# Kernel tuning notes

Hardware: AMD Instinct MI355X
Metric: run time of the kernel (lower is better)

The kernel has to match this reference:

```python
import jax, jax.numpy as jnp
import numpy as np

SHORT = 2000
CUTVALS = [0, 2000, 12000, 40000, 100000]  # [0] + cutoffs + [n_classes]
OSZ = [10000, 28000, 60000]
HSZ = [384, 192, 96]
IN_F = 768
LN_EPS = 1e-5


def setup_inputs() -> dict:
    key = jax.random.key(0)
    ks = jax.random.split(key, 16)
    B, L = 256, 20
    inp = {
        "x": jax.random.normal(ks[0], (B, IN_F), jnp.float32),
        "head_W": jax.random.normal(ks[1], (SHORT + 3, IN_F), jnp.float32) / np.sqrt(IN_F),
        "target": jax.random.randint(ks[2], (B, L), 0, CUTVALS[-1], jnp.int64)
        if jax.config.jax_enable_x64 else jax.random.randint(ks[2], (B, L), 0, CUTVALS[-1], jnp.int32),
    }
    for i in range(3):
        inp[f"w1_{i}"] = jax.random.normal(ks[3 + 4 * i], (HSZ[i], IN_F), jnp.float32) / np.sqrt(IN_F)
        inp[f"g{i}"] = jnp.ones((HSZ[i],), jnp.float32)
        inp[f"b{i}"] = jnp.zeros((HSZ[i],), jnp.float32)
        inp[f"w2_{i}"] = jax.random.normal(ks[4 + 4 * i], (OSZ[i], HSZ[i]), jnp.float32) / np.sqrt(HSZ[i])
    return inp


def _bce_with_logits(logits, y):
    # matches torch BCEWithLogitsLoss(reduction='none')
    return jnp.maximum(logits, 0.0) - logits * y + jnp.log1p(jnp.exp(-jnp.abs(logits)))


def reference(x, head_W, w1_0, g0, b0, w2_0, w1_1, g1, b1, w2_1, w1_2, g2, b2, w2_2, target):
    W1, G, Bp, W2 = [w1_0, w1_1, w1_2], [g0, g1, g2], [b0, b1, b2], [w2_0, w2_1, w2_2]
    B = x.shape[0]
    rows = jnp.arange(B)[:, None]
    dt = x.dtype

    head_logits = x @ head_W.T  # [B, SHORT + n_clusters]

    # shortlist multi-hot (rows with no shortlist label stay all-zero, as in torch)
    m0 = target < SHORT
    onehot_short = jnp.zeros((B, SHORT), dt).at[rows, jnp.clip(target, 0, SHORT - 1)].max(m0.astype(dt))

    total_cluster = jnp.zeros((B,), dt)
    actives = []
    for i in range(3):
        low, high = CUTVALS[i + 1], CUTVALS[i + 2]
        osz = high - low
        m = (target >= low) & (target < high)  # [B, L]
        active = m.any(axis=1).astype(dt)      # [B]
        actives.append(active)
        # multi-hot targets for this cluster
        y = jnp.zeros((B, osz), dt).at[rows, jnp.clip(target - low, 0, osz - 1)].max(m.astype(dt))
        # tail projection: Linear -> LayerNorm -> ReLU -> Linear
        h = x @ W1[i].T
        mu = h.mean(-1, keepdims=True)
        var = ((h - mu) ** 2).mean(-1, keepdims=True)
        h = jax.nn.relu((h - mu) * jax.lax.rsqrt(var + LN_EPS) * G[i] + Bp[i])
        # p = sigmoid(cluster-root logit) * sigmoid(tail logits)
        root = jax.nn.sigmoid(head_logits[:, SHORT + i])[:, None]  # [B,1]
        p = root * jax.nn.sigmoid(h @ W2[i].T)                     # [B, osz]
        # torch BCELoss clamps log at -100
        bce = -(y * jnp.maximum(jnp.log(p), -100.0) + (1.0 - y) * jnp.maximum(jnp.log1p(-p), -100.0))
        total_cluster = total_cluster + active * bce.sum(axis=1)

    cluster_onehot = jnp.stack(actives, axis=1)  # [B, 3]
    head_y = jnp.concatenate([onehot_short, cluster_onehot], axis=1)
    head_loss = _bce_with_logits(head_logits, head_y)  # [B, SHORT+3]
    mult = (cluster_onehot == 0).astype(dt)
    head_loss = jnp.concatenate([head_loss[:, :SHORT], head_loss[:, SHORT:] * mult], axis=1)
    head_loss = head_loss.sum(axis=1)

    csz = jnp.asarray(OSZ, dt)
    num_loss = (mult + cluster_onehot * csz).sum(axis=1) + SHORT
    return ((head_loss + total_cluster) / num_loss).mean()
```

## Files before the change

### kernel.cpp

```cpp
#include <hip/hip_runtime.h>
#include <hip/hip_bf16.h>

#define INF 768
#define NSHORT 2000
#define NHEAD 2003

typedef __attribute__((ext_vector_type(8))) short  s16x8;
typedef __attribute__((ext_vector_type(4))) float  f32x4;
typedef __attribute__((ext_vector_type(8))) float  f32x8;

__device__ __forceinline__ float sigf(float z) { return 1.f / (1.f + __expf(-z)); }
__device__ __forceinline__ float softplusf(float z) {
    return fmaxf(z, 0.f) + __logf(1.f + __expf(-fabsf(z)));
}
__device__ __forceinline__ float qreduce16(float v) {
    v += __shfl_xor(v, 1); v += __shfl_xor(v, 2);
    v += __shfl_xor(v, 4); v += __shfl_xor(v, 8);
    return v;
}
__device__ __forceinline__ float wreduce64(float v) {
    v += __shfl_xor(v, 1);  v += __shfl_xor(v, 2);  v += __shfl_xor(v, 4);
    v += __shfl_xor(v, 8);  v += __shfl_xor(v, 16); v += __shfl_xor(v, 32);
    return v;
}
__device__ __forceinline__ short bfc(float x) {
    union { __hip_bfloat16 h; short s; } u; u.h = __float2bfloat16(x); return u.s;
}

template <int K32, int KC, int MODE, int AF32>
__device__ __forceinline__ void core_c(
    const void* __restrict__ Av, int kbase32,
    const float* __restrict__ W, int Kfull, int N, int stripe,
    short* __restrict__ lds,
    float* __restrict__ outH, int ldH,
    float* __restrict__ part, int pslot,
    const float* __restrict__ rootlogit, int ci)
{
    constexpr int NCH = K32 / KC;
    const int t = threadIdx.x;
    const int wave = t >> 6, lane = t & 63;
    const int quad = lane >> 4, l16 = lane & 15;
    const int rtb = wave * 4;

    const int sct = t >> 6, sl = t & 63;
    int scol = stripe * 64 + sct * 16 + (sl & 15);
    if (scol >= N) scol = N - 1;
    const float* wsrc = W + (size_t)scol * Kfull + kbase32 * 32 + (sl >> 4) * 8;

    size_t aoff[4];
#pragma unroll
    for (int rt = 0; rt < 4; rt++) {
        if (AF32)
            aoff[rt] = (size_t)((rtb + rt) * 16 + l16) * Kfull + kbase32 * 32 + quad * 8;
        else
            aoff[rt] = (size_t)(rtb + rt) * K32 * 512 + (size_t)lane * 8;
    }

#pragma unroll
    for (int s = 0; s < KC; s++) {
        const f32x8 v = *(const f32x8*)(wsrc + (size_t)s * 32);
        s16x8 o;
#pragma unroll
        for (int i = 0; i < 8; i++) o[i] = bfc(v[i]);
        *(s16x8*)(lds + (((size_t)s * 4 + sct) * 64 + sl) * 8) = o;
    }
    __syncthreads();

    f32x4 acc[4][4];
#pragma unroll
    for (int rt = 0; rt < 4; rt++)
#pragma unroll
        for (int ct = 0; ct < 4; ct++) acc[rt][ct] = (f32x4){0.f, 0.f, 0.f, 0.f};

#pragma unroll
    for (int c = 0; c < NCH; c++) {
        short* lbuf = lds + (size_t)(c & 1) * (KC * 2048);
        f32x8 nv[KC];
        if (c + 1 < NCH) {
#pragma unroll
            for (int s = 0; s < KC; s++)
                nv[s] = *(const f32x8*)(wsrc + ((size_t)((c + 1) * KC + s)) * 32);
        }
#pragma unroll
        for (int jj = 0; jj < KC; jj++) {
            const int jg = c * KC + jj;
            s16x8 af[4];
            if (AF32) {
#pragma unroll
                for (int rt = 0; rt < 4; rt++) {
                    const f32x8 v = *(const f32x8*)((const float*)Av + aoff[rt] + (size_t)jg * 32);
#pragma unroll
                    for (int i = 0; i < 8; i++) af[rt][i] = bfc(v[i]);
                }
            } else {
#pragma unroll
                for (int rt = 0; rt < 4; rt++)
                    af[rt] = *(const s16x8*)((const short*)Av + aoff[rt] + (size_t)jg * 512);
            }
#pragma unroll
            for (int ct = 0; ct < 4; ct++) {
                const s16x8 wf = *(const s16x8*)(lbuf + (((size_t)jj * 4 + ct) * 64 + lane) * 8);
#pragma unroll
                for (int rt = 0; rt < 4; rt++)
                    acc[rt][ct] = __builtin_amdgcn_mfma_f32_16x16x32_bf16(
                        af[rt], wf, acc[rt][ct], 0, 0, 0);
            }
        }
        if (c + 1 < NCH) {
            short* nbuf = lds + (size_t)((c + 1) & 1) * (KC * 2048);
            __syncthreads();
#pragma unroll
            for (int s = 0; s < KC; s++) {
                s16x8 o;
#pragma unroll
                for (int i = 0; i < 8; i++) o[i] = bfc(nv[s][i]);
                *(s16x8*)(nbuf + (((size_t)s * 4 + sct) * 64 + sl) * 8) = o;
            }
            __syncthreads();
        }
    }

    const int col0 = stripe * 64;
    if (MODE == 0) {
#pragma unroll
        for (int rt = 0; rt < 4; rt++)
#pragma unroll
            for (int ct = 0; ct < 4; ct++) {
                const int col = col0 + ct * 16 + l16;
                if (col < N) {
#pragma unroll
                    for (int r = 0; r < 4; r++)
                        outH[(size_t)((rtb + rt) * 16 + quad * 4 + r) * ldH + col] =
                            acc[rt][ct][r];
                }
            }
    } else if (MODE == 1) {
#pragma unroll
        for (int rt = 0; rt < 4; rt++) {
#pragma unroll
            for (int r = 0; r < 4; r++) {
                const int row = (rtb + rt) * 16 + quad * 4 + r;
                float m = 0.f, Pp = 1.f;
#pragma unroll
                for (int ct = 0; ct < 4; ct++) {
                    const int col = col0 + ct * 16 + l16;
                    if (col < NSHORT) {
                        const float z = acc[rt][ct][r];
                        m += fmaxf(z, 0.f);
                        Pp *= 1.f + __expf(-fabsf(z));
                    }
                }
                float s = m + __logf(Pp);
                s = qreduce16(s);
                if (l16 == 0) part[(size_t)pslot * 256 + row] = s;
            }
        }
    } else {
#pragma unroll
        for (int rt = 0; rt < 4; rt++) {
#pragma unroll
            for (int r = 0; r < 4; r++) {
                const int row = (rtb + rt) * 16 + quad * 4 + r;
                const float rv = sigf(rootlogit[row * 3 + ci]);
                float pd = 1.f, pn = 1.f;
#pragma unroll
                for (int ct = 0; ct < 4; ct++) {
                    const int col = col0 + ct * 16 + l16;
                    const float tv = fminf(__expf(-acc[rt][ct][r]), 1e6f);
                    const float d = (col < N) ? (1.f + tv) : 1.f;
                    const float n = (col < N) ? (1.f + tv - rv) : 1.f;
                    pd *= d; pn *= n;
                }
                float s = __logf(pd) - __logf(pn);
                s = qreduce16(s);
                if (l16 == 0) part[(size_t)pslot * 256 + row] = s;
            }
        }
    }
}

template <int K32>
__device__ __forceinline__ void core_b(
    const __hip_bfloat16* __restrict__ Ap,
    const float* __restrict__ W, int N, int stripe,
    short* __restrict__ lds,
    float* __restrict__ part, int pslot,
    const float* __restrict__ rootlogit, int ci)
{
    const int t = threadIdx.x;
    const int wave = t >> 6, lane = t & 63;
    const int quad = lane >> 4, l16 = lane & 15;
    const int rtb = wave * 4;
    const int Kfull = K32 * 32;

    const int sct = t >> 6, sl = t & 63;
    int scol = stripe * 64 + sct * 16 + (sl & 15);
    if (scol >= N) scol = N - 1;
    const float* wsrc = W + (size_t)scol * Kfull + (sl >> 4) * 8;
    short* wdst = lds + ((size_t)sct * 64 + sl) * 8;

    constexpr int G = (K32 <= 6) ? K32 : 6;
    constexpr int NG = K32 / G;
    f32x8 buf[G];
#pragma unroll
    for (int s = 0; s < G; s++) buf[s] = *(const f32x8*)(wsrc + (size_t)s * 32);
#pragma unroll
    for (int gg = 0; gg < NG; gg++) {
        f32x8 nbuf[G];
        if (gg + 1 < NG) {
#pragma unroll
            for (int s = 0; s < G; s++)
                nbuf[s] = *(const f32x8*)(wsrc + (size_t)((gg + 1) * G + s) * 32);
        }
#pragma unroll
        for (int s = 0; s < G; s++) {
            s16x8 o;
#pragma unroll
            for (int i = 0; i < 8; i++) o[i] = bfc(buf[s][i]);
            *(s16x8*)(wdst + (size_t)(gg * G + s) * 2048) = o;
        }
        if (gg + 1 < NG) {
#pragma unroll
            for (int s = 0; s < G; s++) buf[s] = nbuf[s];
        }
    }
    __syncthreads();

    const short* abase = (const short*)Ap + (size_t)lane * 8;
    f32x4 acc[4][4];
#pragma unroll
    for (int rt = 0; rt < 4; rt++)
#pragma unroll
        for (int ct = 0; ct < 4; ct++) acc[rt][ct] = (f32x4){0.f, 0.f, 0.f, 0.f};

#pragma unroll
    for (int j = 0; j < K32; j++) {
        s16x8 af[4];
#pragma unroll
        for (int rt = 0; rt < 4; rt++)
            af[rt] = *(const s16x8*)(abase + (size_t)((rtb + rt) * K32 + j) * 512);
#pragma unroll
        for (int ct = 0; ct < 4; ct++) {
            const s16x8 wf = *(const s16x8*)(lds + (((size_t)j * 4 + ct) * 64 + lane) * 8);
#pragma unroll
            for (int rt = 0; rt < 4; rt++)
                acc[rt][ct] = __builtin_amdgcn_mfma_f32_16x16x32_bf16(
                    af[rt], wf, acc[rt][ct], 0, 0, 0);
        }
    }

    const int col0 = stripe * 64;
#pragma unroll
    for (int rt = 0; rt < 4; rt++) {
#pragma unroll
        for (int r = 0; r < 4; r++) {
            const int row = (rtb + rt) * 16 + quad * 4 + r;
            const float rv = sigf(rootlogit[row * 3 + ci]);
            float pd = 1.f, pn = 1.f;
#pragma unroll
            for (int ct = 0; ct < 4; ct++) {
                const int col = col0 + ct * 16 + l16;
                const float tv = fminf(__expf(-acc[rt][ct][r]), 1e6f);
                const float d = (col < N) ? (1.f + tv) : 1.f;
                const float n = (col < N) ? (1.f + tv - rv) : 1.f;
                pd *= d; pn *= n;
            }
            float s = __logf(pd) - __logf(pn);
            s = qreduce16(s);
            if (l16 == 0) part[(size_t)pslot * 256 + row] = s;
        }
    }
}

__global__ __launch_bounds__(256) void k_mm1(
    const float* __restrict__ x, const float* __restrict__ headW,
    const float* __restrict__ w10, const float* __restrict__ w11,
    const float* __restrict__ w12,
    float* __restrict__ phead,
    float* h0, float* h1, float* h2,
    float* __restrict__ rootlogit)
{
    __shared__ __align__(16) short smem[16384];
    const int bx = blockIdx.x;
    if (bx < 32) {
        core_c<24, 4, 1, 1>(x, 0, headW, INF, NHEAD, bx, smem,
                            nullptr, 0, phead, bx, nullptr, 0);
    } else if (bx < 38) {
        core_c<24, 4, 0, 1>(x, 0, w10, INF, 384, bx - 32, smem,
                            h0, 384, nullptr, 0, nullptr, 0);
    } else if (bx < 41) {
        core_c<24, 4, 0, 1>(x, 0, w11, INF, 192, bx - 38, smem,
                            h1, 192, nullptr, 0, nullptr, 0);
    } else if (bx < 43) {
        core_c<24, 4, 0, 1>(x, 0, w12, INF, 96, bx - 41, smem,
                            h2, 96, nullptr, 0, nullptr, 0);
    } else {
        const int row = bx - 43, wave = threadIdx.x >> 6, lane = threadIdx.x & 63;
        if (wave < 3) {
            const float* xr = x + row * INF;
            const float* wr = headW + (size_t)(NSHORT + wave) * INF;
            float s = 0.f;
            for (int k = lane; k < INF; k += 64) s += xr[k] * wr[k];
            s = wreduce64(s);
            if (lane == 0) rootlogit[row * 3 + wave] = s;
        }
    }
}

__global__ __launch_bounds__(256) void k_ln(const float* h0, const float* h1, const float* h2,
                                            const float* g0, const float* g1, const float* g2,
                                            const float* b0, const float* b1, const float* b2,
                                            __hip_bfloat16* f0, __hip_bfloat16* f1,
                                            __hip_bfloat16* f2,
                                            __hip_bfloat16* p0, __hip_bfloat16* p1,
                                            __hip_bfloat16* p2,
                                            float* __restrict__ out) {
    if (blockIdx.x == 0 && threadIdx.x == 0) out[0] = 0.f;
    const int task = blockIdx.x * 4 + (threadIdx.x >> 6);
    const int ci = task >> 8, row = task & 255, lane = threadIdx.x & 63;
    const float *h, *g, *bb; __hip_bfloat16 *fo, *po; int hsz, K32;
    if (ci == 0)      { h = h0; g = g0; bb = b0; fo = f0; po = p0; hsz = 384; K32 = 12; }
    else if (ci == 1) { h = h1; g = g1; bb = b1; fo = f1; po = p1; hsz = 192; K32 = 6; }
    else              { h = h2; g = g2; bb = b2; fo = f2; po = p2; hsz = 96;  K32 = 3; }
    const float* hr = h + (size_t)row * hsz;
    float s = 0.f, s2 = 0.f;
    for (int k = lane; k < hsz; k += 64) { const float v = hr[k]; s += v; s2 += v * v; }
    s = wreduce64(s); s2 = wreduce64(s2);
    const float mu = s / hsz;
    const float var = s2 / hsz - mu * mu;
    const float rsn = rsqrtf(var + 1e-5f);
    const int nch = hsz >> 3;
    if (lane < nch) {
        const f32x8 v = *(const f32x8*)(hr + lane * 8);
        const f32x8 gg = *(const f32x8*)(g + lane * 8);
        const f32x8 bv = *(const f32x8*)(bb + lane * 8);
        s16x8 o;
#pragma unroll
        for (int i = 0; i < 8; i++)
            o[i] = bfc(fmaxf((v[i] - mu) * rsn * gg[i] + bv[i], 0.f));
        *(s16x8*)((short*)fo + (size_t)row * hsz + lane * 8) = o;
        const size_t chunk = ((size_t)(row >> 4) * K32 + (lane >> 2)) * 64
                           + (lane & 3) * 16 + (row & 15);
        *(s16x8*)((short*)po + chunk * 8) = o;
    }
}

__global__ __launch_bounds__(256) void k_bce(const __hip_bfloat16* p0,
                                             const __hip_bfloat16* p1,
                                             const __hip_bfloat16* p2,
                                             const float* __restrict__ w20,
                                             const float* __restrict__ w21,
                                             const float* __restrict__ w22,
                                             float* __restrict__ part,
                                             const float* __restrict__ rootlogit) {
    __shared__ __align__(16) short smem[24576];
    const int s = blockIdx.x;
    if (s < 157)
        core_b<12>(p0, w20, 10000, s, smem, part, s, rootlogit, 0);
    else if (s < 595)
        core_b<6>(p1, w21, 28000, s - 157, smem, part, s, rootlogit, 1);
    else
        core_b<3>(p2, w22, 60000, s - 595, smem, part, s, rootlogit, 2);
}

__global__ __launch_bounds__(256) void k_red(const float* __restrict__ part,
                                             const float* __restrict__ phead,
                                             const float* __restrict__ rootlogit,
                                             const int* __restrict__ target,
                                             const float* __restrict__ x,
                                             const float* __restrict__ headW,
                                             const __hip_bfloat16* f0,
                                             const __hip_bfloat16* f1,
                                             const __hip_bfloat16* f2,
                                             const float* w20, const float* w21, const float* w22,
                                             float* __restrict__ out) {
    const int row = blockIdx.x;
    const int t = threadIdx.x, wave = t >> 6, lane = t & 63;
    __shared__ float sx[INF];
    __shared__ __hip_bfloat16 shb[384 + 192 + 96];
    __shared__ int st[20];
    __shared__ float scorr[4];
    __shared__ float red[4][4];
    for (int i = t; i < INF; i += 256) sx[i] = x[row * INF + i];
    for (int i = t; i < 384; i += 256) shb[i] = f0[row * 384 + i];
    for (int i = t; i < 192; i += 256) shb[384 + i] = f1[row * 192 + i];
    for (int i = t; i < 96; i += 256)  shb[576 + i] = f2[row * 96 + i];
    if (t < 20) st[t] = target[row * 20 + t];
    if (t < 4) scorr[t] = 0.f;
    __syncthreads();
    for (int l = wave; l < 20; l += 4) {
        const int tg = st[l];
        bool dup = false;
        for (int m = 0; m < l; m++) dup |= (st[m] == tg);
        if (dup) continue;
        if (tg < NSHORT) {
            const float* wr = headW + (size_t)tg * INF;
            float z = 0.f;
            for (int k = lane; k < INF; k += 64) z += sx[k] * wr[k];
            z = wreduce64(z);
            if (lane == 0) atomicAdd(&scorr[3], -z);
        } else {
            int ci, low, hsz, hoff; const float* w2;
            if (tg < 12000)      { ci = 0; low = 2000;  hsz = 384; hoff = 0;   w2 = w20; }
            else if (tg < 40000) { ci = 1; low = 12000; hsz = 192; hoff = 384; w2 = w21; }
            else                 { ci = 2; low = 40000; hsz = 96;  hoff = 576; w2 = w22; }
            const float* wr = w2 + (size_t)(tg - low) * hsz;
            float z = 0.f;
            for (int k = lane; k < hsz; k += 64)
                z += __bfloat162float(shb[hoff + k]) * wr[k];
            z = wreduce64(z);
            if (lane == 0) {
                const float rvv = sigf(rootlogit[row * 3 + ci]);
                const float p = rvv * sigf(z);
                atomicAdd(&scorr[ci],
                          -fmaxf(__logf(p), -100.f) + fmaxf(__logf(1.f - p), -100.f));
            }
        }
    }
    float c0 = 0.f, c1 = 0.f, c2 = 0.f, hs = 0.f;
    for (int i = t; i < 1533; i += 256) {
        const float v = part[(size_t)i * 256 + row];
        if (i < 157) c0 += v; else if (i < 595) c1 += v; else c2 += v;
    }
    if (t < 32) hs = phead[(size_t)t * 256 + row];
    c0 = wreduce64(c0); c1 = wreduce64(c1); c2 = wreduce64(c2); hs = wreduce64(hs);
    if (lane == 0) { red[0][wave] = c0; red[1][wave] = c1; red[2][wave] = c2; red[3][wave] = hs; }
    __syncthreads();
    if (t == 0) {
        float cc[3];
        for (int i = 0; i < 3; i++) cc[i] = red[i][0] + red[i][1] + red[i][2] + red[i][3];
        float hsum = red[3][0] + red[3][1] + red[3][2] + red[3][3] + scorr[3];
        bool act[3] = {false, false, false};
        for (int l = 0; l < 20; l++) {
            const int tg = target[row * 20 + l];
            if (tg >= 2000) {
                if (tg < 12000) act[0] = true;
                else if (tg < 40000) act[1] = true;
                else act[2] = true;
            }
        }
        float total = 0.f, num = 2000.f;
        const float csz[3] = {10000.f, 28000.f, 60000.f};
        for (int i = 0; i < 3; i++) {
            if (act[i]) { total += cc[i] + scorr[i]; num += csz[i]; }
            else        { hsum += softplusf(rootlogit[row * 3 + i]); num += 1.f; }
        }
        atomicAdd(out, (hsum + total) / num * (1.f / 256.f));
    }
}

extern "C" void kernel_launch(void* const* d_in, const int* in_sizes, int n_in,
                              void* d_out, int out_size, void* d_ws, size_t ws_size,
                              hipStream_t stream) {
    const float* x      = (const float*)d_in[0];
    const float* headW  = (const float*)d_in[1];
    const int*   target = (const int*)d_in[2];
    const float* w10 = (const float*)d_in[3];
    const float* g0  = (const float*)d_in[4];
    const float* b0  = (const float*)d_in[5];
    const float* w20 = (const float*)d_in[6];
    const float* w11 = (const float*)d_in[7];
    const float* g1  = (const float*)d_in[8];
    const float* b1  = (const float*)d_in[9];
    const float* w21 = (const float*)d_in[10];
    const float* w12 = (const float*)d_in[11];
    const float* g2  = (const float*)d_in[12];
    const float* b2  = (const float*)d_in[13];
    const float* w22 = (const float*)d_in[14];
    float* out = (float*)d_out;

    char* ws = (char*)d_ws;
    size_t off = 0;
    auto carve = [&](size_t bytes) -> void* {
        void* p = ws + off;
        off += (bytes + 255) & ~(size_t)255;
        return p;
    };
    float* h0            = (float*)carve((size_t)256 * 384 * 4);
    float* h1            = (float*)carve((size_t)256 * 192 * 4);
    float* h2            = (float*)carve((size_t)256 * 96 * 4);
    __hip_bfloat16* f0   = (__hip_bfloat16*)carve((size_t)256 * 384 * 2);
    __hip_bfloat16* f1   = (__hip_bfloat16*)carve((size_t)256 * 192 * 2);
    __hip_bfloat16* f2   = (__hip_bfloat16*)carve((size_t)256 * 96 * 2);
    __hip_bfloat16* p0   = (__hip_bfloat16*)carve((size_t)256 * 384 * 2);
    __hip_bfloat16* p1   = (__hip_bfloat16*)carve((size_t)256 * 192 * 2);
    __hip_bfloat16* p2   = (__hip_bfloat16*)carve((size_t)256 * 96 * 2);
    float* rootlogit     = (float*)carve((size_t)256 * 3 * 4);
    float* phead         = (float*)carve((size_t)32 * 256 * 4);
    float* part          = (float*)carve((size_t)1536 * 256 * 4);

    k_mm1<<<299, 256, 0, stream>>>(x, headW, w10, w11, w12,
                                   phead, h0, h1, h2, rootlogit);
    k_ln<<<192, 256, 0, stream>>>(h0, h1, h2, g0, g1, g2, b0, b1, b2,
                                  f0, f1, f2, p0, p1, p2, out);
    k_bce<<<1533, 256, 0, stream>>>(p0, p1, p2, w20, w21, w22, part, rootlogit);
    k_red<<<256, 256, 0, stream>>>(part, phead, rootlogit, target, x, headW,
                                   f0, f1, f2, w20, w21, w22, out);

    (void)in_sizes; (void)n_in; (void)out_size; (void)ws_size;
}
```

Measured before the change: 219.9 us.

## Route tail BCE GEMM through pipelined core_c with smaller LDS footprint

Drops the specialized core_b routine and runs the three tail-cluster GEMM+BCE stripes through the generic core_c template, which appears to stage the W2 weights through LDS in K-chunks rather than loading each stripe's full K range up front. The LDS buffer shrinks from 48 KB to 16 KB and launch bounds now request 4 blocks per CU, so more blocks can be resident and weight loads can overlap with MFMA work. The cost is chunked staging overhead and tighter register limits, which could cause spills.

```diff
diff --git a/kernel.cpp b/kernel.cpp
--- a/kernel.cpp
+++ b/kernel.cpp
@@ -175,99 +175,6 @@
                 s = qreduce16(s);
                 if (l16 == 0) part[(size_t)pslot * 256 + row] = s;
             }
-        }
-    }
-}
-
-template <int K32>
-__device__ __forceinline__ void core_b(
-    const __hip_bfloat16* __restrict__ Ap,
-    const float* __restrict__ W, int N, int stripe,
-    short* __restrict__ lds,
-    float* __restrict__ part, int pslot,
-    const float* __restrict__ rootlogit, int ci)
-{
-    const int t = threadIdx.x;
-    const int wave = t >> 6, lane = t & 63;
-    const int quad = lane >> 4, l16 = lane & 15;
-    const int rtb = wave * 4;
-    const int Kfull = K32 * 32;
-
-    const int sct = t >> 6, sl = t & 63;
-    int scol = stripe * 64 + sct * 16 + (sl & 15);
-    if (scol >= N) scol = N - 1;
-    const float* wsrc = W + (size_t)scol * Kfull + (sl >> 4) * 8;
-    short* wdst = lds + ((size_t)sct * 64 + sl) * 8;
-
-    constexpr int G = (K32 <= 6) ? K32 : 6;
-    constexpr int NG = K32 / G;
-    f32x8 buf[G];
-#pragma unroll
-    for (int s = 0; s < G; s++) buf[s] = *(const f32x8*)(wsrc + (size_t)s * 32);
-#pragma unroll
-    for (int gg = 0; gg < NG; gg++) {
-        f32x8 nbuf[G];
-        if (gg + 1 < NG) {
-#pragma unroll
-            for (int s = 0; s < G; s++)
-                nbuf[s] = *(const f32x8*)(wsrc + (size_t)((gg + 1) * G + s) * 32);
-        }
-#pragma unroll
-        for (int s = 0; s < G; s++) {
-            s16x8 o;
-#pragma unroll
-            for (int i = 0; i < 8; i++) o[i] = bfc(buf[s][i]);
-            *(s16x8*)(wdst + (size_t)(gg * G + s) * 2048) = o;
-        }
-        if (gg + 1 < NG) {
-#pragma unroll
-            for (int s = 0; s < G; s++) buf[s] = nbuf[s];
-        }
-    }
-    __syncthreads();
-
-    const short* abase = (const short*)Ap + (size_t)lane * 8;
-    f32x4 acc[4][4];
-#pragma unroll
-    for (int rt = 0; rt < 4; rt++)
-#pragma unroll
-        for (int ct = 0; ct < 4; ct++) acc[rt][ct] = (f32x4){0.f, 0.f, 0.f, 0.f};
-
-#pragma unroll
-    for (int j = 0; j < K32; j++) {
-        s16x8 af[4];
-#pragma unroll
-        for (int rt = 0; rt < 4; rt++)
-            af[rt] = *(const s16x8*)(abase + (size_t)((rtb + rt) * K32 + j) * 512);
-#pragma unroll
-        for (int ct = 0; ct < 4; ct++) {
-            const s16x8 wf = *(const s16x8*)(lds + (((size_t)j * 4 + ct) * 64 + lane) * 8);
-#pragma unroll
-            for (int rt = 0; rt < 4; rt++)
-                acc[rt][ct] = __builtin_amdgcn_mfma_f32_16x16x32_bf16(
-                    af[rt], wf, acc[rt][ct], 0, 0, 0);
-        }
-    }
-
-    const int col0 = stripe * 64;
-#pragma unroll
-    for (int rt = 0; rt < 4; rt++) {
-#pragma unroll
-        for (int r = 0; r < 4; r++) {
-            const int row = (rtb + rt) * 16 + quad * 4 + r;
-            const float rv = sigf(rootlogit[row * 3 + ci]);
-            float pd = 1.f, pn = 1.f;
-#pragma unroll
-            for (int ct = 0; ct < 4; ct++) {
-                const int col = col0 + ct * 16 + l16;
-                const float tv = fminf(__expf(-acc[rt][ct][r]), 1e6f);
-                const float d = (col < N) ? (1.f + tv) : 1.f;
-                const float n = (col < N) ? (1.f + tv - rv) : 1.f;
-                pd *= d; pn *= n;
-            }
-            float s = __logf(pd) - __logf(pn);
-            s = qreduce16(s);
-            if (l16 == 0) part[(size_t)pslot * 256 + row] = s;
         }
     }
 }
@@ -345,22 +252,25 @@
     }
 }
 
-__global__ __launch_bounds__(256) void k_bce(const __hip_bfloat16* p0,
-                                             const __hip_bfloat16* p1,
-                                             const __hip_bfloat16* p2,
-                                             const float* __restrict__ w20,
-                                             const float* __restrict__ w21,
-                                             const float* __restrict__ w22,
-                                             float* __restrict__ part,
-                                             const float* __restrict__ rootlogit) {
-    __shared__ __align__(16) short smem[24576];
+__global__ __launch_bounds__(256, 4) void k_bce(const __hip_bfloat16* p0,
+                                                const __hip_bfloat16* p1,
+                                                const __hip_bfloat16* p2,
+                                                const float* __restrict__ w20,
+                                                const float* __restrict__ w21,
+                                                const float* __restrict__ w22,
+                                                float* __restrict__ part,
+                                                const float* __restrict__ rootlogit) {
+    __shared__ __align__(16) short smem[8192];
     const int s = blockIdx.x;
     if (s < 157)
-        core_b<12>(p0, w20, 10000, s, smem, part, s, rootlogit, 0);
+        core_c<12, 2, 2, 0>(p0, 0, w20, 384, 10000, s, smem,
+                            nullptr, 0, part, s, rootlogit, 0);
     else if (s < 595)
-        core_b<6>(p1, w21, 28000, s - 157, smem, part, s, rootlogit, 1);
+        core_c<6, 2, 2, 0>(p1, 0, w21, 192, 28000, s - 157, smem,
+                           nullptr, 0, part, s, rootlogit, 1);
     else
-        core_b<3>(p2, w22, 60000, s - 595, smem, part, s, rootlogit, 2);
+        core_c<3, 3, 2, 0>(p2, 0, w22, 96, 60000, s - 595, smem,
+                           nullptr, 0, part, s, rootlogit, 2);
 }
 
 __global__ __launch_bounds__(256) void k_red(const float* __restrict__ part,
```

Result: faster. 207.1 us (-5.9%).
